# Performance work log

Hardware: AMD Instinct MI355X
Metric: run time of the kernel (lower is better)

Reference implementation:

```python
import jax, jax.numpy as jnp
import numpy as np

BN_EPS = 1e-5


def _pixel_shuffle(t, r):
    # torch F.pixel_shuffle: [B, C*r^2, H, W] -> [B, C, H*r, W*r]
    B, Cr2, H, W = t.shape
    C = Cr2 // (r * r)
    t = t.reshape(B, C, r, r, H, W)
    t = t.transpose(0, 1, 4, 2, 5, 3)  # B, C, H, r, W, r
    return t.reshape(B, C, H * r, W * r)


def _upsample_bilinear(x, s):
    # F.interpolate(scale_factor=s, mode='bilinear', align_corners=False)
    B, C, H, W = x.shape

    def axis(n_in):
        n_out = n_in * s
        c = (jnp.arange(n_out, dtype=x.dtype) + 0.5) / s - 0.5
        c = jnp.clip(c, 0.0, n_in - 1)
        i0 = jnp.floor(c).astype(jnp.int32)
        i1 = jnp.minimum(i0 + 1, n_in - 1)
        w = c - i0.astype(x.dtype)
        return i0, i1, w

    y0, y1, wy = axis(H)
    x0, x1, wx = axis(W)
    rows = x[:, :, y0, :] * (1.0 - wy)[None, None, :, None] + x[:, :, y1, :] * wy[None, None, :, None]
    out = rows[:, :, :, x0] * (1.0 - wx)[None, None, None, :] + rows[:, :, :, x1] * wx[None, None, None, :]
    return out


def _grid_sample(x, grid):
    # F.grid_sample bilinear, padding_mode='zeros', align_corners=False
    # x: [B,C,H,W], grid: [B,Ho,Wo,2] with (gx, gy) in [-1,1]
    B, C, H, W = x.shape
    gx, gy = grid[..., 0], grid[..., 1]
    ix = ((gx + 1.0) * W - 1.0) * 0.5
    iy = ((gy + 1.0) * H - 1.0) * 0.5
    ix0 = jnp.floor(ix).astype(jnp.int32)
    iy0 = jnp.floor(iy).astype(jnp.int32)
    ix1, iy1 = ix0 + 1, iy0 + 1
    wx1 = ix - ix0.astype(x.dtype)
    wy1 = iy - iy0.astype(x.dtype)
    wx0, wy0 = 1.0 - wx1, 1.0 - wy1

    xf = x.reshape(B, C, H * W)

    def gather(iy_, ix_):
        valid = ((iy_ >= 0) & (iy_ < H) & (ix_ >= 0) & (ix_ < W)).astype(x.dtype)
        idx = jnp.clip(iy_, 0, H - 1) * W + jnp.clip(ix_, 0, W - 1)  # [B,Ho,Wo]
        flat = idx.reshape(B, 1, -1)
        v = jnp.take_along_axis(xf, jnp.broadcast_to(flat, (B, C, flat.shape[-1])), axis=2)
        return v.reshape(B, C, *idx.shape[1:]) * valid[:, None]

    out = (gather(iy0, ix0) * (wy0 * wx0)[:, None]
           + gather(iy0, ix1) * (wy0 * wx1)[:, None]
           + gather(iy1, ix0) * (wy1 * wx0)[:, None]
           + gather(iy1, ix1) * (wy1 * wx1)[:, None])
    return out


def _conv1x1(x, w, b=None):
    y = jnp.einsum('bchw,oc->bohw', x, w)
    if b is not None:
        y = y + b[None, :, None, None]
    return y


def _forward(x, offset_w, offset_b, mask_w, mask_b, conv_w, bn_gamma, bn_beta, bn_mean, bn_var, s):
    B, C, H, W = x.shape
    x_up = _upsample_bilinear(x, s)
    offset = _conv1x1(x, offset_w, offset_b)              # [B, 2*s*s, H, W]
    mask = jax.nn.sigmoid(_conv1x1(x, mask_w, mask_b))    # [B, s*s, H, W]
    offset = _pixel_shuffle(offset, s)                    # [B, 2, H*s, W*s]
    mask = _pixel_shuffle(mask, s)                        # [B, 1, H*s, W*s]
    Hs, Ws = H * s, W * s
    gy = jnp.linspace(-1.0, 1.0, Hs, dtype=x.dtype)
    gx = jnp.linspace(-1.0, 1.0, Ws, dtype=x.dtype)
    GX, GY = jnp.meshgrid(gx, gy)                         # 'xy': GX[h,w]=gx[w], GY[h,w]=gy[h]
    base_grid = jnp.stack((GX, GY), axis=-1)              # [Hs, Ws, 2]
    grid = base_grid[None] + offset.transpose(0, 2, 3, 1)
    sampled = _grid_sample(x_up, grid)
    out = sampled * mask
    y = _conv1x1(out, conv_w)
    y = (y - bn_mean[None, :, None, None]) * jax.lax.rsqrt(bn_var[None, :, None, None] + BN_EPS)
    y = y * bn_gamma[None, :, None, None] + bn_beta[None, :, None, None]
    return y * jax.nn.sigmoid(y)  # SiLU


def setup_inputs() -> dict:
    key = jax.random.key(0)
    ks = jax.random.split(key, 8)
    B, C, H, W, s = 16, 64, 80, 80, 2
    f = jnp.float32
    x = jax.random.normal(ks[0], (B, C, H, W), f)
    offset_w = jax.random.normal(ks[1], (2 * s * s, C), f) * 0.05
    offset_b = jax.random.normal(ks[2], (2 * s * s,), f) * 0.05
    mask_w = jax.random.normal(ks[3], (s * s, C), f) * 0.1
    mask_b = jnp.zeros((s * s,), f)
    conv_w = jax.random.normal(ks[4], (C, C), f) * (1.0 / np.sqrt(C))
    bn_gamma = jnp.ones((C,), f)
    bn_beta = jnp.zeros((C,), f)
    bn_mean = jax.random.normal(ks[5], (C,), f) * 0.1
    bn_var = jax.random.uniform(ks[6], (C,), f, 0.5, 1.5)
    return {"x": x, "offset_w": offset_w, "offset_b": offset_b, "mask_w": mask_w,
            "mask_b": mask_b, "conv_w": conv_w, "bn_gamma": bn_gamma, "bn_beta": bn_beta,
            "bn_mean": bn_mean, "bn_var": bn_var, "scale": 2}


def reference(x, offset_w, offset_b, mask_w, mask_b, conv_w, bn_gamma, bn_beta, bn_mean, bn_var, scale):
    return _forward(x, offset_w, offset_b, mask_w, mask_b, conv_w, bn_gamma, bn_beta, bn_mean, bn_var, scale)
```

## Files before the change

### kernel.cpp

```cpp
#include <hip/hip_runtime.h>

typedef unsigned short ushort_t;
typedef __attribute__((ext_vector_type(8))) short bf16x8;
typedef __attribute__((ext_vector_type(4))) float f32x4;

__device__ __forceinline__ float bf2f(ushort_t u) {
    union { unsigned int i; float f; } v; v.i = ((unsigned int)u) << 16; return v.f;
}
__device__ __forceinline__ ushort_t f2bf(float f) {
    union { float f; unsigned int i; } v; v.f = f;
    unsigned int r = v.i + 0x7FFFu + ((v.i >> 16) & 1u);
    return (ushort_t)(r >> 16);
}

#define BB 16
#define CC 64
#define HH 80
#define WW 80
#define HS 160
#define WS 160
#define HW (HH*WW)
#define HWS (HS*WS)

__global__ void prep_params(const float* __restrict__ offset_w,
                            const float* __restrict__ offset_b,
                            const float* __restrict__ mask_w,
                            const float* __restrict__ mask_b,
                            const float* __restrict__ conv_w,
                            const float* __restrict__ gamma,
                            const float* __restrict__ beta,
                            const float* __restrict__ mean,
                            const float* __restrict__ var,
                            float* __restrict__ wmat, float* __restrict__ wbias,
                            ushort_t* __restrict__ cwBf,
                            float* __restrict__ bnA, float* __restrict__ bnB) {
    int t = threadIdx.x;
    for (int i = t; i < 12 * 64; i += 256) {
        int ch = i >> 6, c = i & 63;
        wmat[i] = ch < 8 ? offset_w[ch * 64 + c] : mask_w[(ch - 8) * 64 + c];
    }
    if (t < 12) wbias[t] = t < 8 ? offset_b[t] : mask_b[t - 8];
    for (int i = t; i < 64 * 64; i += 256) cwBf[i] = f2bf(conv_w[i]);
    if (t < 64) {
        float A = gamma[t] * rsqrtf(var[t] + 1e-5f);
        bnA[t] = A;
        bnB[t] = beta[t] - mean[t] * A;
    }
}

__global__ __launch_bounds__(256) void prep_x(const float* __restrict__ x,
                                              const float* __restrict__ wmat,
                                              const float* __restrict__ wbias,
                                              ushort_t* __restrict__ xT,
                                              float* __restrict__ offs) {
    __shared__ float sX[64 * 65];
    int t = threadIdx.x;
    int tile = blockIdx.x;
    int b = tile / 100;
    int hw0 = (tile - b * 100) * 64;
    const float* xb = x + (size_t)b * CC * HW + hw0;

#pragma unroll
    for (int k = 0; k < 4; ++k) {
        int e = k * 256 + t;
        int c = e >> 4, j4 = (e & 15) << 2;
        f32x4 v = *(const f32x4*)(xb + (size_t)c * HW + j4);
        sX[(j4 + 0) * 65 + c] = v.x;
        sX[(j4 + 1) * 65 + c] = v.y;
        sX[(j4 + 2) * 65 + c] = v.z;
        sX[(j4 + 3) * 65 + c] = v.w;
    }
    __syncthreads();

    size_t xtb = ((size_t)(b * HW) + hw0) * CC;
#pragma unroll
    for (int k = 0; k < 4; ++k) {
        int e = k * 256 + t;
        int j = e >> 4, c4 = (e & 15) << 2;
        const float* rp = sX + j * 65 + c4;
        unsigned int u0 = (unsigned int)f2bf(rp[0]) | ((unsigned int)f2bf(rp[1]) << 16);
        unsigned int u1 = (unsigned int)f2bf(rp[2]) | ((unsigned int)f2bf(rp[3]) << 16);
        unsigned int* dst = (unsigned int*)(xT + xtb + (size_t)j * CC + c4);
        dst[0] = u0;
        dst[1] = u1;
    }

    int px = t & 63;
    int chunk = __builtin_amdgcn_readfirstlane(t >> 6);
    int ch0 = chunk * 3;
    const float* w0 = wmat + (ch0 + 0) * 64;
    const float* w1 = wmat + (ch0 + 1) * 64;
    const float* w2 = wmat + (ch0 + 2) * 64;
    float a0 = 0.f, a1 = 0.f, a2 = 0.f;
#pragma unroll 4
    for (int c = 0; c < 64; ++c) {
        float v = sX[px * 65 + c];
        a0 += v * w0[c];
        a1 += v * w1[c];
        a2 += v * w2[c];
    }
    a0 += wbias[ch0 + 0];
    a1 += wbias[ch0 + 1];
    a2 += wbias[ch0 + 2];
    if (ch0 + 0 >= 8) a0 = 1.0f / (1.0f + __expf(-a0));
    if (ch0 + 1 >= 8) a1 = 1.0f / (1.0f + __expf(-a1));
    if (ch0 + 2 >= 8) a2 = 1.0f / (1.0f + __expf(-a2));
    float* op = offs + (size_t)(b * HW + hw0 + px) * 12;
    op[ch0 + 0] = a0;
    op[ch0 + 1] = a1;
    op[ch0 + 2] = a2;
}

#define ACC3(w, k, val) { float _v = (val); \
    w[0] += (k) == 0 ? _v : 0.f; w[1] += (k) == 1 ? _v : 0.f; w[2] += (k) == 2 ? _v : 0.f; }

__device__ __forceinline__ void axis_taps(float pos, int& base, float w[3]) {
    float f = floorf(pos); int u0 = (int)f; float g1 = pos - f;
    w[0] = w[1] = w[2] = 0.f;
    bool v0 = (u0 >= 0) & (u0 < 160);
    bool v1 = (u0 + 1 >= 0) & (u0 + 1 < 160);
    float cc0 = 0.f, cc1 = 0.f; int ca0 = 0, ca1 = 0;
    if (v0) { cc0 = fminf(fmaxf((float)u0 * 0.5f - 0.25f, 0.f), 79.f); ca0 = (int)floorf(cc0); }
    if (v1) { cc1 = fminf(fmaxf((float)(u0 + 1) * 0.5f - 0.25f, 0.f), 79.f); ca1 = (int)floorf(cc1); }
    int first = v0 ? ca0 : (v1 ? ca1 : 0);
    base = min(first, 77);
    if (v0) {
        float wv = cc0 - (float)ca0; int c1 = min(ca0 + 1, 79);
        int k0 = ca0 - base, k1 = c1 - base;
        ACC3(w, k0, (1.f - g1) * (1.f - wv));
        ACC3(w, k1, (1.f - g1) * wv);
    }
    if (v1) {
        float wv = cc1 - (float)ca1; int c1 = min(ca1 + 1, 79);
        int k0 = ca1 - base, k1 = c1 - base;
        ACC3(w, k0, g1 * (1.f - wv));
        ACC3(w, k1, g1 * wv);
    }
}

__global__ __launch_bounds__(256) void dysample_main(const ushort_t* __restrict__ xT,
                                                     const float* __restrict__ offs,
                                                     const ushort_t* __restrict__ cwBf,
                                                     const float* __restrict__ bnA,
                                                     const float* __restrict__ bnB,
                                                     float* __restrict__ out) {
    __shared__ float sTap[64 * 8];
    __shared__ ushort_t S[64 * 72];
    int t = threadIdx.x;
    int lane = t & 63;
    int wave = __builtin_amdgcn_readfirstlane(t >> 6);
    int quad = lane >> 4, nrow = lane & 15;
    int b = blockIdx.y;
    int pix0 = blockIdx.x * 64;

    const ushort_t* wp = cwBf + (wave * 16 + nrow) * 64 + quad * 8;
    bf16x8 af0 = *(const bf16x8*)(wp);
    bf16x8 af1 = *(const bf16x8*)(wp + 32);
    int coutD = wave * 16 + quad * 4;
    float bnAv[4], bnBv[4];
#pragma unroll
    for (int j = 0; j < 4; ++j) { bnAv[j] = bnA[coutD + j]; bnBv[j] = bnB[coutD + j]; }

    if (t < 64) {
        int pix = pix0 + t;
        int ho = pix / WS, wo = pix - ho * WS;
        int h = ho >> 1, w = wo >> 1, r = ((ho & 1) << 1) | (wo & 1);
        const float* op = offs + (size_t)((b * HW) + h * WW + w) * 12;
        float ox = op[r], oy = op[4 + r], mk = op[8 + r];
        float ix = (float)wo * (160.0f / 159.0f) - 0.5f + 80.0f * ox;
        float iy = (float)ho * (160.0f / 159.0f) - 0.5f + 80.0f * oy;
        int cb, rb; float cw[3], rw[3];
        axis_taps(ix, cb, cw);
        axis_taps(iy, rb, rw);
        sTap[t * 8 + 0] = __int_as_float(cb | (rb << 16));
        sTap[t * 8 + 1] = cw[0]; sTap[t * 8 + 2] = cw[1]; sTap[t * 8 + 3] = cw[2];
        sTap[t * 8 + 4] = rw[0]; sTap[t * 8 + 5] = rw[1]; sTap[t * 8 + 6] = rw[2];
        sTap[t * 8 + 7] = mk;
    }
    __syncthreads();

    const ushort_t* xb = xT + (size_t)b * HW * CC;
#pragma unroll 2
    for (int i = 0; i < 16; ++i) {
        int px = wave * 16 + i;
        f32x4 t0 = *(const f32x4*)(sTap + px * 8);
        f32x4 t1 = *(const f32x4*)(sTap + px * 8 + 4);
        int bits = __float_as_int(t0.x);
        int cb = bits & 0xffff, rb = bits >> 16;
        const ushort_t* p0 = xb + (rb * WW + cb) * CC + lane;
        float acc = 0.f;
#pragma unroll
        for (int rr = 0; rr < 3; ++rr) {
            const ushort_t* pr = p0 + rr * (WW * CC);
            float v0 = bf2f(pr[0]);
            float v1 = bf2f(pr[64]);
            float v2 = bf2f(pr[128]);
            float rowa = t0.y * v0 + t0.z * v1 + t0.w * v2;
            float rwv = (rr == 0) ? t1.x : ((rr == 1) ? t1.y : t1.z);
            acc += rwv * rowa;
        }
        S[px * 72 + lane] = f2bf(acc * t1.w);
    }
    __syncthreads();

    f32x4 acc4[4];
#pragma unroll
    for (int n = 0; n < 4; ++n) acc4[n] = (f32x4){0.f, 0.f, 0.f, 0.f};
#pragma unroll
    for (int n = 0; n < 4; ++n) {
        const ushort_t* sp = S + (n * 16 + nrow) * 72 + quad * 8;
        bf16x8 b0 = *(const bf16x8*)(sp);
        bf16x8 b1 = *(const bf16x8*)(sp + 32);
        acc4[n] = __builtin_amdgcn_mfma_f32_16x16x32_bf16(af0, b0, acc4[n], 0, 0, 0);
        acc4[n] = __builtin_amdgcn_mfma_f32_16x16x32_bf16(af1, b1, acc4[n], 0, 0, 0);
    }

    size_t ob = (size_t)b * CC * HWS;
#pragma unroll
    for (int n = 0; n < 4; ++n) {
        int pix = pix0 + n * 16 + nrow;
#pragma unroll
        for (int j = 0; j < 4; ++j) {
            float y = acc4[n][j] * bnAv[j] + bnBv[j];
            float s = y / (1.0f + __expf(-y));
            out[ob + (size_t)(coutD + j) * HWS + pix] = s;
        }
    }
}

extern "C" void kernel_launch(void* const* d_in, const int* in_sizes, int n_in,
                              void* d_out, int out_size, void* d_ws, size_t ws_size,
                              hipStream_t stream) {
    const float* x        = (const float*)d_in[0];
    const float* offset_w = (const float*)d_in[1];
    const float* offset_b = (const float*)d_in[2];
    const float* mask_w   = (const float*)d_in[3];
    const float* mask_b   = (const float*)d_in[4];
    const float* conv_w   = (const float*)d_in[5];
    const float* bn_gamma = (const float*)d_in[6];
    const float* bn_beta  = (const float*)d_in[7];
    const float* bn_mean  = (const float*)d_in[8];
    const float* bn_var   = (const float*)d_in[9];

    char* ws = (char*)d_ws;
    size_t off = 0;
    ushort_t* xT   = (ushort_t*)(ws + off); off += (size_t)BB * HW * CC * 2;
    float*    offs = (float*)(ws + off);    off += (size_t)BB * HW * 12 * 4;
    ushort_t* cwBf = (ushort_t*)(ws + off); off += 64 * 64 * 2;
    float*    wmat = (float*)(ws + off);    off += 12 * 64 * 4;
    float*    wbias= (float*)(ws + off);    off += 64;
    float*    bnA  = (float*)(ws + off);    off += 64 * 4;
    float*    bnB  = (float*)(ws + off);    off += 64 * 4;

    prep_params<<<1, 256, 0, stream>>>(offset_w, offset_b, mask_w, mask_b, conv_w,
                                       bn_gamma, bn_beta, bn_mean, bn_var,
                                       wmat, wbias, cwBf, bnA, bnB);
    prep_x<<<BB * (HW / 64), 256, 0, stream>>>(x, wmat, wbias, xT, offs);
    dysample_main<<<dim3(HWS / 64, BB), 256, 0, stream>>>(xT, offs, cwBf, bnA, bnB,
                                                          (float*)d_out);
}
```

Baseline: 190.4 us.

## Store transposed x as fp32 and gather 8 channels per lane with vector loads

The channel-last copy of x is now kept in fp32 instead of bf16, and the sampling stage has each lane handle 8 contiguous channels of one pixel through 128-bit loads, writing a packed bf16x8 to shared memory. The aim is fewer, wider gather instructions in place of many scalar 2-byte loads. In exchange the intermediate buffer doubles in size, which adds write and read traffic in both kernels.

```diff
diff --git a/kernel.cpp b/kernel.cpp
--- a/kernel.cpp
+++ b/kernel.cpp
@@ -51,7 +51,7 @@
 __global__ __launch_bounds__(256) void prep_x(const float* __restrict__ x,
                                               const float* __restrict__ wmat,
                                               const float* __restrict__ wbias,
-                                              ushort_t* __restrict__ xT,
+                                              float* __restrict__ xT,
                                               float* __restrict__ offs) {
     __shared__ float sX[64 * 65];
     int t = threadIdx.x;
@@ -78,11 +78,8 @@
         int e = k * 256 + t;
         int j = e >> 4, c4 = (e & 15) << 2;
         const float* rp = sX + j * 65 + c4;
-        unsigned int u0 = (unsigned int)f2bf(rp[0]) | ((unsigned int)f2bf(rp[1]) << 16);
-        unsigned int u1 = (unsigned int)f2bf(rp[2]) | ((unsigned int)f2bf(rp[3]) << 16);
-        unsigned int* dst = (unsigned int*)(xT + xtb + (size_t)j * CC + c4);
-        dst[0] = u0;
-        dst[1] = u1;
+        f32x4 v = {rp[0], rp[1], rp[2], rp[3]};
+        *(f32x4*)(xT + xtb + (size_t)j * CC + c4) = v;
     }
 
     int px = t & 63;
@@ -138,7 +135,7 @@
     }
 }
 
-__global__ __launch_bounds__(256) void dysample_main(const ushort_t* __restrict__ xT,
+__global__ __launch_bounds__(256) void dysample_main(const float* __restrict__ xT,
                                                      const float* __restrict__ offs,
                                                      const ushort_t* __restrict__ cwBf,
                                                      const float* __restrict__ bnA,
@@ -179,27 +176,41 @@
     }
     __syncthreads();
 
-    const ushort_t* xb = xT + (size_t)b * HW * CC;
-#pragma unroll 2
-    for (int i = 0; i < 16; ++i) {
-        int px = wave * 16 + i;
+    int sub8 = lane >> 3;
+    int g8 = (lane & 7) << 3;
+    const float* xb = xT + (size_t)b * HW * CC;
+#pragma unroll
+    for (int i = 0; i < 2; ++i) {
+        int px = wave * 16 + i * 8 + sub8;
         f32x4 t0 = *(const f32x4*)(sTap + px * 8);
         f32x4 t1 = *(const f32x4*)(sTap + px * 8 + 4);
         int bits = __float_as_int(t0.x);
         int cb = bits & 0xffff, rb = bits >> 16;
-        const ushort_t* p0 = xb + (rb * WW + cb) * CC + lane;
-        float acc = 0.f;
+        const float* p0 = xb + (size_t)(rb * WW + cb) * CC + g8;
+        float acc[8];
+#pragma unroll
+        for (int j = 0; j < 8; ++j) acc[j] = 0.f;
 #pragma unroll
         for (int rr = 0; rr < 3; ++rr) {
-            const ushort_t* pr = p0 + rr * (WW * CC);
-            float v0 = bf2f(pr[0]);
-            float v1 = bf2f(pr[64]);
-            float v2 = bf2f(pr[128]);
-            float rowa = t0.y * v0 + t0.z * v1 + t0.w * v2;
+            const float* pr = p0 + rr * (WW * CC);
             float rwv = (rr == 0) ? t1.x : ((rr == 1) ? t1.y : t1.z);
-            acc += rwv * rowa;
+            float w0 = rwv * t0.y, w1 = rwv * t0.z, w2 = rwv * t0.w;
+            f32x4 c0a = *(const f32x4*)(pr);
+            f32x4 c0b = *(const f32x4*)(pr + 4);
+            f32x4 c1a = *(const f32x4*)(pr + CC);
+            f32x4 c1b = *(const f32x4*)(pr + CC + 4);
+            f32x4 c2a = *(const f32x4*)(pr + 2 * CC);
+            f32x4 c2b = *(const f32x4*)(pr + 2 * CC + 4);
+#pragma unroll
+            for (int j = 0; j < 4; ++j) {
+                acc[j]     += w0 * c0a[j] + w1 * c1a[j] + w2 * c2a[j];
+                acc[j + 4] += w0 * c0b[j] + w1 * c1b[j] + w2 * c2b[j];
+            }
         }
-        S[px * 72 + lane] = f2bf(acc * t1.w);
+        bf16x8 outv;
+#pragma unroll
+        for (int j = 0; j < 8; ++j) outv[j] = (short)f2bf(acc[j] * t1.w);
+        *(bf16x8*)(S + px * 72 + g8) = outv;
     }
     __syncthreads();
 
@@ -244,7 +255,7 @@
 
     char* ws = (char*)d_ws;
     size_t off = 0;
-    ushort_t* xT   = (ushort_t*)(ws + off); off += (size_t)BB * HW * CC * 2;
+    float*    xT   = (float*)(ws + off);    off += (size_t)BB * HW * CC * 4;
     float*    offs = (float*)(ws + off);    off += (size_t)BB * HW * 12 * 4;
     ushort_t* cwBf = (ushort_t*)(ws + off); off += 64 * 64 * 2;
     float*    wmat = (float*)(ws + off);    off += 12 * 64 * 4;
```

New measurement: 211.6 us. 1.11x slower.

## Vectorize 3x3 tap gathers with 16-byte loads and swizzle block order

Applied to the files above, without the earlier changes.

The gather stage changes from one bf16 scalar load per lane per tap over 16 serial pixels to 16-byte bf16x8 loads. Each group of 8 lanes handles one pixel's 64 channels, and all 18 tap loads are issued up front for two pixels per lane. This raises memory-level parallelism and cuts the number of load instructions. Separately, blockIdx.x is remapped so consecutive blocks are spread across 8 strided groups of 50, which changes the L2/MALL locality pattern. In exchange it raises register pressure from holding 18 vector loads, and the block remap assumes exactly 400 blocks in x.

```diff
diff --git a/kernel.cpp b/kernel.cpp
--- a/kernel.cpp
+++ b/kernel.cpp
@@ -151,7 +151,9 @@
     int wave = __builtin_amdgcn_readfirstlane(t >> 6);
     int quad = lane >> 4, nrow = lane & 15;
     int b = blockIdx.y;
-    int pix0 = blockIdx.x * 64;
+    int bx = blockIdx.x;
+    int lx = ((bx & 7) * 50) + (bx >> 3);
+    int pix0 = lx * 64;
 
     const ushort_t* wp = cwBf + (wave * 16 + nrow) * 64 + quad * 8;
     bf16x8 af0 = *(const bf16x8*)(wp);
@@ -179,27 +181,75 @@
     }
     __syncthreads();
 
+    int sub8 = lane >> 3;
+    int g8 = (lane & 7) << 3;
     const ushort_t* xb = xT + (size_t)b * HW * CC;
-#pragma unroll 2
-    for (int i = 0; i < 16; ++i) {
-        int px = wave * 16 + i;
-        f32x4 t0 = *(const f32x4*)(sTap + px * 8);
-        f32x4 t1 = *(const f32x4*)(sTap + px * 8 + 4);
-        int bits = __float_as_int(t0.x);
-        int cb = bits & 0xffff, rb = bits >> 16;
-        const ushort_t* p0 = xb + (rb * WW + cb) * CC + lane;
-        float acc = 0.f;
-#pragma unroll
-        for (int rr = 0; rr < 3; ++rr) {
-            const ushort_t* pr = p0 + rr * (WW * CC);
-            float v0 = bf2f(pr[0]);
-            float v1 = bf2f(pr[64]);
-            float v2 = bf2f(pr[128]);
-            float rowa = t0.y * v0 + t0.z * v1 + t0.w * v2;
-            float rwv = (rr == 0) ? t1.x : ((rr == 1) ? t1.y : t1.z);
-            acc += rwv * rowa;
+
+    int pxA = wave * 16 + sub8;
+    int pxB = wave * 16 + 8 + sub8;
+    f32x4 tA0 = *(const f32x4*)(sTap + pxA * 8);
+    f32x4 tA1 = *(const f32x4*)(sTap + pxA * 8 + 4);
+    f32x4 tB0 = *(const f32x4*)(sTap + pxB * 8);
+    f32x4 tB1 = *(const f32x4*)(sTap + pxB * 8 + 4);
+    int bitsA = __float_as_int(tA0.x);
+    int cbA = bitsA & 0xffff, rbA = bitsA >> 16;
+    int bitsB = __float_as_int(tB0.x);
+    int cbB = bitsB & 0xffff, rbB = bitsB >> 16;
+    const ushort_t* pA = xb + (rbA * WW + cbA) * CC + g8;
+    const ushort_t* pB = xb + (rbB * WW + cbB) * CC + g8;
+
+    bf16x8 a00 = *(const bf16x8*)(pA);
+    bf16x8 a01 = *(const bf16x8*)(pA + CC);
+    bf16x8 a02 = *(const bf16x8*)(pA + 2 * CC);
+    bf16x8 a10 = *(const bf16x8*)(pA + WW * CC);
+    bf16x8 a11 = *(const bf16x8*)(pA + WW * CC + CC);
+    bf16x8 a12 = *(const bf16x8*)(pA + WW * CC + 2 * CC);
+    bf16x8 a20 = *(const bf16x8*)(pA + 2 * WW * CC);
+    bf16x8 a21 = *(const bf16x8*)(pA + 2 * WW * CC + CC);
+    bf16x8 a22 = *(const bf16x8*)(pA + 2 * WW * CC + 2 * CC);
+    bf16x8 b00 = *(const bf16x8*)(pB);
+    bf16x8 b01 = *(const bf16x8*)(pB + CC);
+    bf16x8 b02 = *(const bf16x8*)(pB + 2 * CC);
+    bf16x8 b10 = *(const bf16x8*)(pB + WW * CC);
+    bf16x8 b11 = *(const bf16x8*)(pB + WW * CC + CC);
+    bf16x8 b12 = *(const bf16x8*)(pB + WW * CC + 2 * CC);
+    bf16x8 b20 = *(const bf16x8*)(pB + 2 * WW * CC);
+    bf16x8 b21 = *(const bf16x8*)(pB + 2 * WW * CC + CC);
+    bf16x8 b22 = *(const bf16x8*)(pB + 2 * WW * CC + 2 * CC);
+
+    {
+        float w00 = tA1.x * tA0.y, w01 = tA1.x * tA0.z, w02 = tA1.x * tA0.w;
+        float w10 = tA1.y * tA0.y, w11 = tA1.y * tA0.z, w12 = tA1.y * tA0.w;
+        float w20 = tA1.z * tA0.y, w21 = tA1.z * tA0.z, w22 = tA1.z * tA0.w;
+        bf16x8 outv;
+#pragma unroll
+        for (int j = 0; j < 8; ++j) {
+            float a = w00 * bf2f((ushort_t)a00[j]) + w01 * bf2f((ushort_t)a01[j])
+                    + w02 * bf2f((ushort_t)a02[j])
+                    + w10 * bf2f((ushort_t)a10[j]) + w11 * bf2f((ushort_t)a11[j])
+                    + w12 * bf2f((ushort_t)a12[j])
+                    + w20 * bf2f((ushort_t)a20[j]) + w21 * bf2f((ushort_t)a21[j])
+                    + w22 * bf2f((ushort_t)a22[j]);
+            outv[j] = (short)f2bf(a * tA1.w);
         }
-        S[px * 72 + lane] = f2bf(acc * t1.w);
+        *(bf16x8*)(S + pxA * 72 + g8) = outv;
+    }
+    {
+        float w00 = tB1.x * tB0.y, w01 = tB1.x * tB0.z, w02 = tB1.x * tB0.w;
+        float w10 = tB1.y * tB0.y, w11 = tB1.y * tB0.z, w12 = tB1.y * tB0.w;
+        float w20 = tB1.z * tB0.y, w21 = tB1.z * tB0.z, w22 = tB1.z * tB0.w;
+        bf16x8 outv;
+#pragma unroll
+        for (int j = 0; j < 8; ++j) {
+            float a = w00 * bf2f((ushort_t)b00[j]) + w01 * bf2f((ushort_t)b01[j])
+                    + w02 * bf2f((ushort_t)b02[j])
+                    + w10 * bf2f((ushort_t)b10[j]) + w11 * bf2f((ushort_t)b11[j])
+                    + w12 * bf2f((ushort_t)b12[j])
+                    + w20 * bf2f((ushort_t)b20[j]) + w21 * bf2f((ushort_t)b21[j])
+                    + w22 * bf2f((ushort_t)b22[j]);
+            outv[j] = (short)f2bf(a * tB1.w);
+        }
+        *(bf16x8*)(S + pxB * 72 + g8) = outv;
     }
     __syncthreads();
 
```

Result: faster. 178.2 us (-6.4%).
